# Kernel tuning notes

Measured on AMD Instinct MI355X. Metric: run time of the kernel, lower is better.

## Reference

```python
import math
import jax, jax.numpy as jnp
import numpy as np

B, N, T, C, H = 16, 307, 24, 128, 8
D = C // H
FACTOR = 5
S = min(FACTOR * int(np.ceil(np.log(T))), T)   # sample_k (U_part) = 20
U = S                                          # n_top u = 20


def _pos_emb(t_len, c):
    pos = jnp.arange(t_len, dtype=jnp.float32)[:, None]
    div = jnp.exp(jnp.arange(0, c, 2, dtype=jnp.float32) * (-math.log(10000.0) / c))
    pe = jnp.zeros((t_len, c), dtype=jnp.float32)
    pe = pe.at[:, 0::2].set(jnp.sin(pos * div))
    pe = pe.at[:, 1::2].set(jnp.cos(pos * div))
    return pe  # [T, C]


def _layernorm(x, g, b, eps=1e-5):
    m = x.mean(-1, keepdims=True)
    v = ((x - m) ** 2).mean(-1, keepdims=True)
    return (x - m) / jnp.sqrt(v + eps) * g + b


def _forward(query, time_encoder, index_sample,
             emb_minute, emb_hour, emb_weekday, emb_month, emb_year,
             Wq, Wk, Wv, Wo, bo, ff_w1, ff_b1, ff_w2, ff_b2,
             ln1_g, ln1_b, ln2_g, ln2_b):
    # DataEmbedding: x + positional + temporal (dropout = identity in eval)
    pe = _pos_emb(T, C)                                   # [T, C]
    te = (emb_minute[time_encoder[..., 0]] + emb_hour[time_encoder[..., 1]]
          + emb_weekday[time_encoder[..., 2]] + emb_month[time_encoder[..., 3]]
          + emb_year[time_encoder[..., 4]])               # [B, T, C]
    x = query + pe[None, None, :, :] + te[:, None, :, :]  # [B, N, T, C]

    # QKV projections -> [B, H, N, T, D]
    def proj(inp, W):
        return (inp @ W).reshape(B, N, T, H, D).transpose(0, 3, 1, 2, 4)
    Q, K, V = proj(x, Wq), proj(x, Wk), proj(x, Wv)

    # ProbSparse: sample S keys per query position
    K_samp = K[:, :, :, index_sample, :]                  # [B, H, N, T, S, D]
    QK_samp = jnp.einsum('bhntd,bhntsd->bhnts', Q, K_samp)
    M = QK_samp.max(-1) - QK_samp.sum(-1) / S             # [B, H, N, T]
    _, M_top = jax.lax.top_k(M, U)                        # [B, H, N, U]

    Q_red = jnp.take_along_axis(Q, M_top[..., None], axis=3)  # [B, H, N, U, D]
    scores = jnp.einsum('bhnud,bhntd->bhnut', Q_red, K) * (1.0 / math.sqrt(D))
    attn = jax.nn.softmax(scores, axis=-1)
    upd = jnp.einsum('bhnut,bhntd->bhnud', attn, V)       # [B, H, N, U, D]

    # initial context = mean over T, then scatter-update top-u query rows
    ctx = jnp.broadcast_to(V.mean(axis=3, keepdims=True), V.shape)
    ctx = ctx.at[jnp.arange(B)[:, None, None, None],
                 jnp.arange(H)[None, :, None, None],
                 jnp.arange(N)[None, None, :, None],
                 M_top].set(upd)

    ctx = ctx.transpose(0, 2, 3, 1, 4).reshape(B, N, T, C)
    att_out = ctx @ Wo + bo

    x1 = _layernorm(att_out + x, ln1_g, ln1_b)
    ff = jax.nn.relu(x1 @ ff_w1 + ff_b1) @ ff_w2 + ff_b2
    out = _layernorm(ff + x1, ln2_g, ln2_b)
    return out


def setup_inputs() -> dict:
    key = jax.random.key(0)
    ks = jax.random.split(key, 32)
    def nrm(i, shape, s=0.02):
        return jax.random.normal(ks[i], shape, dtype=jnp.float32) * s
    inp = {
        'value': jax.random.normal(ks[0], (B, N, T, C), dtype=jnp.float32),
        'key_in': jax.random.normal(ks[1], (B, N, T, C), dtype=jnp.float32),
        'query': jax.random.normal(ks[2], (B, N, T, C), dtype=jnp.float32),
        't': 1,
        'time_encoder': jax.random.randint(ks[3], (B, T, 5), 0, 10),
        'index_sample': jax.random.randint(ks[4], (T, S), 0, T),
        'emb_minute': nrm(5, (70, C), 1.0), 'emb_hour': nrm(6, (30, C), 1.0),
        'emb_weekday': nrm(7, (10, C), 1.0), 'emb_month': nrm(8, (40, C), 1.0),
        'emb_year': nrm(9, (400, C), 1.0),
        'Wq': nrm(10, (C, C)), 'Wk': nrm(11, (C, C)), 'Wv': nrm(12, (C, C)),
        'Wo': nrm(13, (C, C)), 'bo': jnp.zeros((C,), jnp.float32),
        'ff_w1': nrm(14, (C, 4 * C)), 'ff_b1': jnp.zeros((4 * C,), jnp.float32),
        'ff_w2': nrm(15, (4 * C, C)), 'ff_b2': jnp.zeros((C,), jnp.float32),
        'ln1_g': jnp.ones((C,), jnp.float32), 'ln1_b': jnp.zeros((C,), jnp.float32),
        'ln2_g': jnp.ones((C,), jnp.float32), 'ln2_b': jnp.zeros((C,), jnp.float32),
    }
    return inp


def reference(value, key_in, query, t, time_encoder, index_sample,
              emb_minute, emb_hour, emb_weekday, emb_month, emb_year,
              Wq, Wk, Wv, Wo, bo, ff_w1, ff_b1, ff_w2, ff_b2,
              ln1_g, ln1_b, ln2_g, ln2_b):
    # value, key_in, t are accepted but unused, matching the torch module
    return _forward(query, time_encoder, index_sample,
                    emb_minute, emb_hour, emb_weekday, emb_month, emb_year,
                    Wq, Wk, Wv, Wo, bo, ff_w1, ff_b1, ff_w2, ff_b2,
                    ln1_g, ln1_b, ln2_g, ln2_b)
```

## Files before the change

kernel.cpp:

```cpp
#include <hip/hip_runtime.h>
#include <hip/hip_bf16.h>
#include <cmath>

namespace {
constexpr int B_ = 16, N_ = 307, T_ = 24, C_ = 128, H_ = 8, D_ = 16, S_ = 20, U_ = 20;
constexpr int NROW = B_ * N_ * T_;
constexpr int NX = NROW * C_;
constexpr int TEPE_N = B_ * T_ * C_;
constexpr int FF = 4 * C_;
constexpr int BM = 32;
constexpr int NBLK_MM = NROW / BM;
constexpr int BMT = 32;
constexpr int NBLK_T = NROW / BMT;
constexpr int NUNIT = B_ * H_ * N_;
constexpr int PREP_N = TEPE_N + 384 * C_ + (2 * C_ * FF + C_ * C_);
}

typedef __attribute__((ext_vector_type(8))) short short8;
typedef __attribute__((ext_vector_type(4))) short short4_;
typedef __attribute__((ext_vector_type(4))) float f32x4;

__device__ inline short f2bf(float v) {
    union { float f; unsigned u; } a; a.f = v;
    unsigned r = a.u + 0x7fff + ((a.u >> 16) & 1);
    return (short)(r >> 16);
}
__device__ inline float bf2f(short s) {
    return __bfloat162float(*(const __hip_bfloat16*)&s);
}

__global__ void k_prep(const int* __restrict__ te,
                       const float* __restrict__ e_min, const float* __restrict__ e_hr,
                       const float* __restrict__ e_wd, const float* __restrict__ e_mo,
                       const float* __restrict__ e_yr, float* __restrict__ tepe,
                       const int* __restrict__ idxs, unsigned char* __restrict__ cntg,
                       const float* __restrict__ Wq, const float* __restrict__ Wk,
                       const float* __restrict__ Wv, short* __restrict__ wqkvf,
                       const float* __restrict__ w1, const float* __restrict__ w2,
                       const float* __restrict__ Wo,
                       short* __restrict__ w1f, short* __restrict__ w2f,
                       short* __restrict__ wof) {
    int i = blockIdx.x * 256 + threadIdx.x;
    if (i < TEPE_N) {
        int c = i & (C_ - 1);
        int bt = i >> 7;
        int t = bt % T_;
        const int* enc = te + bt * 5;
        float v = e_min[enc[0] * C_ + c] + e_hr[enc[1] * C_ + c] + e_wd[enc[2] * C_ + c]
                + e_mo[enc[3] * C_ + c] + e_yr[enc[4] * C_ + c];
        float ang = (float)t * expf(-(float)(c & ~1) * (9.210340371976184f / 128.0f));
        v += (c & 1) ? cosf(ang) : sinf(ang);
        tepe[i] = v;
    } else if (i < TEPE_N + 384 * C_) {
        int j = i - TEPE_N;
        int tile = j >> 9, l = (j >> 3) & 63, e = j & 7;
        int c_tile = tile >> 2, ks = tile & 3;
        int c_all = c_tile * 16 + (l & 15);
        int k = ks * 32 + (l >> 4) * 8 + e;
        int m = c_all >> 7, c = c_all & (C_ - 1);
        const float* W = (m == 0) ? Wq : (m == 1) ? Wk : Wv;
        wqkvf[j] = f2bf(W[k * C_ + c]);
    } else {
        int j = i - TEPE_N - 384 * C_;
        if (j < C_ * FF) {
            int tile = j >> 9, l = (j >> 3) & 63, e = j & 7;
            int jtile = tile >> 2, ks = tile & 3;
            int jj = jtile * 16 + (l & 15);
            int k = ks * 32 + (l >> 4) * 8 + e;
            w1f[j] = f2bf(w1[k * FF + jj]);
        } else if (j < 2 * C_ * FF) {
            int j2 = j - C_ * FF;
            int tile = j2 >> 9, l = (j2 >> 3) & 63, e = j2 & 7;
            int c_tile = tile >> 4, ks = tile & 15;
            int c = c_tile * 16 + (l & 15);
            int jj = ks * 32 + (l >> 4) * 8 + e;
            w2f[j2] = f2bf(w2[jj * C_ + c]);
        } else {
            int j3 = j - 2 * C_ * FF;
            int tile = j3 >> 9, l = (j3 >> 3) & 63, e = j3 & 7;
            int c_tile = tile >> 2, ks = tile & 3;
            int c = c_tile * 16 + (l & 15);
            int k = ks * 32 + (l >> 4) * 8 + e;
            wof[j3] = f2bf(Wo[k * C_ + c]);
        }
    }
    if (blockIdx.x == 0) {
        __shared__ int scnt[T_ * 32];
        for (int j = threadIdx.x; j < T_ * 32; j += 256) scnt[j] = 0;
        __syncthreads();
        for (int j = threadIdx.x; j < T_ * S_; j += 256) {
            int t = j / S_;
            atomicAdd(&scnt[t * 32 + idxs[j]], 1);
        }
        __syncthreads();
        for (int j = threadIdx.x; j < 192; j += 256) {
            unsigned v = (unsigned)scnt[4 * j] | ((unsigned)scnt[4 * j + 1] << 8)
                       | ((unsigned)scnt[4 * j + 2] << 16) | ((unsigned)scnt[4 * j + 3] << 24);
            ((unsigned*)cntg)[j] = v;
        }
    }
}

__global__ __launch_bounds__(256) void k_qkv_mfma(
    const float* __restrict__ query, const float* __restrict__ tepe,
    const short* __restrict__ wqkvf,
    short* __restrict__ Q, short* __restrict__ K, short* __restrict__ V) {
    __shared__ __align__(16) short xs[BM * C_];
    int tid = threadIdx.x;
    int r0 = blockIdx.x * BM;
    {
        int row = tid >> 3;
        int cb = (tid & 7) * 16;
        int gr = r0 + row;
        int t = gr % T_;
        int b = gr / (N_ * T_);
        const float* qsrc = query + (size_t)gr * C_ + cb;
        const float* tsrc = tepe + (size_t)(b * T_ + t) * C_ + cb;
        int swz0 = (row & 7) << 3;
#pragma unroll
        for (int i = 0; i < 4; i++) {
            float4 q4 = *(const float4*)(qsrc + 4 * i);
            float4 t4 = *(const float4*)(tsrc + 4 * i);
            short4_ sv;
            sv.x = f2bf(q4.x + t4.x); sv.y = f2bf(q4.y + t4.y);
            sv.z = f2bf(q4.z + t4.z); sv.w = f2bf(q4.w + t4.w);
            *(short4_*)&xs[(row * C_ + cb + 4 * i) ^ swz0] = sv;
        }
    }
    __syncthreads();
    int w = tid >> 6, l = tid & 63;
    int lr = l & 15, lk = l >> 4;
    int swz = (lr & 7) << 3;
    short8 bx[2][4];
#pragma unroll
    for (int rt = 0; rt < 2; rt++)
#pragma unroll
        for (int ks = 0; ks < 4; ks++)
            bx[rt][ks] = *(const short8*)&xs[((rt * 16 + lr) * C_ + ks * 32 + lk * 8) ^ swz];
    size_t base[2];
#pragma unroll
    for (int rt = 0; rt < 2; rt++) {
        int gr = r0 + rt * 16 + lr;
        int t = gr % T_;
        int n = (gr / T_) % N_;
        int b = gr / (N_ * T_);
        base[rt] = ((size_t)b * H_ * N_ + n) * (T_ * D_) + t * D_;
    }
#pragma unroll
    for (int jt = 0; jt < 6; jt++) {
        int ctile = w * 6 + jt;
        const short* ap = wqkvf + (size_t)ctile * 2048 + l * 8;
        short8 acur[4];
#pragma unroll
        for (int ks = 0; ks < 4; ks++) acur[ks] = *(const short8*)(ap + ks * 512);
        f32x4 acc[2] = {{0.f, 0.f, 0.f, 0.f}, {0.f, 0.f, 0.f, 0.f}};
#pragma unroll
        for (int ks = 0; ks < 4; ks++) {
#pragma unroll
            for (int rt = 0; rt < 2; rt++)
                acc[rt] = __builtin_amdgcn_mfma_f32_16x16x32_bf16(acur[ks], bx[rt][ks], acc[rt], 0, 0, 0);
        }
        int c0 = ctile * 16 + lk * 4;
        int m = c0 >> 7;
        int c = c0 & (C_ - 1);
        int h = c >> 4, d = c & 15;
        short* dst = (m == 0) ? Q : (m == 1) ? K : V;
#pragma unroll
        for (int rt = 0; rt < 2; rt++) {
            short4_ sv;
            sv.x = f2bf(acc[rt][0]); sv.y = f2bf(acc[rt][1]);
            sv.z = f2bf(acc[rt][2]); sv.w = f2bf(acc[rt][3]);
            *(short4_*)&dst[base[rt] + (size_t)h * (N_ * T_ * D_) + d] = sv;
        }
    }
}

__global__ __launch_bounds__(256) void k_attn(
    const short* __restrict__ Q, const short* __restrict__ K, const short* __restrict__ V,
    const unsigned char* __restrict__ cntg, short* __restrict__ ctx) {
    __shared__ __align__(16) short Qbf[4][32 * 24], Kbf[4][32 * 24];
    __shared__ __align__(16) short Vt[4][16 * 40];
    __shared__ __align__(16) short Pbf[4][32 * 40];
    __shared__ unsigned char cntS[T_ * 32];
    __shared__ float Mv[4][T_];
    __shared__ int keepS[4][T_];
    __shared__ float meanVs[4][D_];
    int tid = threadIdx.x;
    int wid = tid >> 6, l = tid & 63;
    int e = blockIdx.x * 4 + wid;
    const short* qb = Q + (size_t)e * (T_ * D_);
    const short* kb = K + (size_t)e * (T_ * D_);
    const short* vb = V + (size_t)e * (T_ * D_);
    if (l < 48) {
        int t = l >> 1, hf = l & 1;
        *(short8*)&Qbf[wid][t * 24 + hf * 8] = *(const short8*)(qb + t * 16 + hf * 8);
        *(short8*)&Kbf[wid][t * 24 + hf * 8] = *(const short8*)(kb + t * 16 + hf * 8);
    }
    for (int i = l; i < 96; i += 64) {
        int t = i >> 2, c4 = i & 3;
        short4_ v = *(const short4_*)(vb + t * 16 + c4 * 4);
        Vt[wid][(c4 * 4 + 0) * 40 + t] = v.x;
        Vt[wid][(c4 * 4 + 1) * 40 + t] = v.y;
        Vt[wid][(c4 * 4 + 2) * 40 + t] = v.z;
        Vt[wid][(c4 * 4 + 3) * 40 + t] = v.w;
    }
    for (int i = l; i < 128; i += 64) {
        int d = i >> 3, c = 24 + (i & 7);
        Vt[wid][d * 40 + c] = 0;
    }
    if (tid < 192) ((int*)cntS)[tid] = ((const int*)cntg)[tid];
    __syncthreads();
    if (l >= 48) {
        int d = l - 48;
        float s = 0.f;
        for (int t = 0; t < T_; t++) s += bf2f(Vt[wid][d * 40 + t]);
        meanVs[wid][d] = s * (1.0f / T_);
    }
    int lr = l & 15, lk = l >> 4;
    short8 zz = {};
    short8 kf0 = zz, kf1 = zz, qf0 = zz, qf1 = zz;
    if (lk < 2) {
        kf0 = *(const short8*)&Kbf[wid][lr * 24 + lk * 8];
        kf1 = *(const short8*)&Kbf[wid][(16 + lr) * 24 + lk * 8];
        qf0 = *(const short8*)&Qbf[wid][lr * 24 + lk * 8];
        qf1 = *(const short8*)&Qbf[wid][(16 + lr) * 24 + lk * 8];
    }
    f32x4 zf = {0.f, 0.f, 0.f, 0.f};
    __builtin_amdgcn_s_setprio(1);
    f32x4 s00 = __builtin_amdgcn_mfma_f32_16x16x32_bf16(kf0, qf0, zf, 0, 0, 0);
    f32x4 s01 = __builtin_amdgcn_mfma_f32_16x16x32_bf16(kf1, qf0, zf, 0, 0, 0);
    f32x4 s10 = __builtin_amdgcn_mfma_f32_16x16x32_bf16(kf0, qf1, zf, 0, 0, 0);
    f32x4 s11 = __builtin_amdgcn_mfma_f32_16x16x32_bf16(kf1, qf1, zf, 0, 0, 0);
    __builtin_amdgcn_s_setprio(0);
#pragma unroll
    for (int rt = 0; rt < 2; rt++) {
        int t = rt * 16 + lr;
        int tt = (t < T_) ? t : 0;
        f32x4 c0 = rt ? s10 : s00;
        f32x4 c1 = rt ? s11 : s01;
        float mx = -1e30f, sm = 0.f;
#pragma unroll
        for (int i = 0; i < 4; i++) {
            int cA = cntS[tt * 32 + lk * 4 + i];
            if (cA) { mx = fmaxf(mx, c0[i]); sm += (float)cA * c0[i]; }
        }
        if (lk < 2) {
#pragma unroll
            for (int i = 0; i < 4; i++) {
                int cB = cntS[tt * 32 + 16 + lk * 4 + i];
                if (cB) { mx = fmaxf(mx, c1[i]); sm += (float)cB * c1[i]; }
            }
        }
        mx = fmaxf(mx, __shfl_xor(mx, 16));
        mx = fmaxf(mx, __shfl_xor(mx, 32));
        sm += __shfl_xor(sm, 16);
        sm += __shfl_xor(sm, 32);
        if (lk == 0 && t < T_) Mv[wid][t] = mx - sm * (1.0f / S_);
    }
    __syncthreads();
    if (l < T_) {
        float mt = Mv[wid][l];
        int cnt2 = 0;
        for (int t2 = 0; t2 < T_; t2++) {
            float m2 = Mv[wid][t2];
            cnt2 += (m2 > mt) || (m2 == mt && t2 < l);
        }
        keepS[wid][l] = (cnt2 < U_) ? 1 : 0;
    }
#pragma unroll
    for (int rt = 0; rt < 2; rt++) {
        f32x4 c0 = rt ? s10 : s00;
        f32x4 c1 = rt ? s11 : s01;
        float lm = fmaxf(fmaxf(c0[0], c0[1]), fmaxf(c0[2], c0[3]));
        if (lk < 2) lm = fmaxf(lm, fmaxf(fmaxf(c1[0], c1[1]), fmaxf(c1[2], c1[3])));
        lm = fmaxf(lm, __shfl_xor(lm, 16));
        lm = fmaxf(lm, __shfl_xor(lm, 32));
        float e0[4], e1[4];
        float ls = 0.f;
#pragma unroll
        for (int i = 0; i < 4; i++) { e0[i] = __expf(0.25f * (c0[i] - lm)); ls += e0[i]; }
#pragma unroll
        for (int i = 0; i < 4; i++) { e1[i] = (lk < 2) ? __expf(0.25f * (c1[i] - lm)) : 0.f; ls += e1[i]; }
        ls += __shfl_xor(ls, 16);
        ls += __shfl_xor(ls, 32);
        float inv = 1.0f / ls;
        short4_ w0, w1;
        w0.x = f2bf(e0[0] * inv); w0.y = f2bf(e0[1] * inv);
        w0.z = f2bf(e0[2] * inv); w0.w = f2bf(e0[3] * inv);
        w1.x = f2bf(e1[0] * inv); w1.y = f2bf(e1[1] * inv);
        w1.z = f2bf(e1[2] * inv); w1.w = f2bf(e1[3] * inv);
        int trow = rt * 16 + lr;
        *(short4_*)&Pbf[wid][trow * 40 + lk * 4] = w0;
        *(short4_*)&Pbf[wid][trow * 40 + 16 + lk * 4] = w1;
    }
    __syncthreads();
    short8 vf = *(const short8*)&Vt[wid][lr * 40 + lk * 8];
    short8 pf0 = *(const short8*)&Pbf[wid][lr * 40 + lk * 8];
    short8 pf1 = *(const short8*)&Pbf[wid][(16 + lr) * 40 + lk * 8];
    __builtin_amdgcn_s_setprio(1);
    f32x4 u0 = __builtin_amdgcn_mfma_f32_16x16x32_bf16(vf, pf0, zf, 0, 0, 0);
    f32x4 u1 = __builtin_amdgcn_mfma_f32_16x16x32_bf16(vf, pf1, zf, 0, 0, 0);
    __builtin_amdgcn_s_setprio(0);
    int b = e / (H_ * N_);
    int h = (e / N_) % H_;
    int n = e % N_;
    float4 mv4 = *(const float4*)&meanVs[wid][lk * 4];
#pragma unroll
    for (int rt = 0; rt < 2; rt++) {
        int t = rt * 16 + lr;
        if (t < T_) {
            f32x4 u = rt ? u1 : u0;
            float4 o;
            if (keepS[wid][t]) { o.x = u[0]; o.y = u[1]; o.z = u[2]; o.w = u[3]; }
            else o = mv4;
            short4_ sv;
            sv.x = f2bf(o.x); sv.y = f2bf(o.y); sv.z = f2bf(o.z); sv.w = f2bf(o.w);
            *(short4_*)&ctx[((size_t)(b * N_ + n) * T_ + t) * C_ + h * D_ + lk * 4] = sv;
        }
    }
}

__global__ __launch_bounds__(256, 4) void k_tail(
    const short* __restrict__ ctx, const short* __restrict__ wof, const float* __restrict__ bo,
    const float* __restrict__ query, const float* __restrict__ tepe,
    const float* __restrict__ g1, const float* __restrict__ b1,
    const short* __restrict__ w1f, const float* __restrict__ b1f,
    const short* __restrict__ w2f, const float* __restrict__ b2f,
    const float* __restrict__ g2, const float* __restrict__ b2ln,
    float* __restrict__ out) {
    __shared__ __align__(16) char smem[25088];
    float (*xf)[132] = (float(*)[132])smem;
    short* hbf = (short*)smem;
    float (*yf)[132] = (float(*)[132])smem;
    short* cbf = (short*)(smem + 16896);
    short* x1bf = (short*)(smem + 16896);
    int tid = threadIdx.x;
    int r0 = blockIdx.x * BMT;
    {
        int row = tid >> 3;
        int cb = (tid & 7) * 16;
        int gr = r0 + row;
        int t = gr % T_;
        int b = gr / (N_ * T_);
        const short* csrc = ctx + (size_t)gr * C_ + cb;
        const float* qsrc = query + (size_t)gr * C_ + cb;
        const float* tsrc = tepe + (size_t)(b * T_ + t) * C_ + cb;
        int swz0 = (row & 7) << 3;
        *(short8*)&cbf[(row * C_ + cb) ^ swz0] = *(const short8*)csrc;
        *(short8*)&cbf[(row * C_ + cb + 8) ^ swz0] = *(const short8*)(csrc + 8);
#pragma unroll
        for (int i = 0; i < 4; i++) {
            float4 q4 = *(const float4*)(qsrc + 4 * i);
            float4 t4 = *(const float4*)(tsrc + 4 * i);
            float4 xr;
            xr.x = q4.x + t4.x; xr.y = q4.y + t4.y;
            xr.z = q4.z + t4.z; xr.w = q4.w + t4.w;
            *(float4*)&xf[row][cb + 4 * i] = xr;
        }
    }
    __syncthreads();
    int w = tid >> 6, l = tid & 63;
    int lr = l & 15, lk = l >> 4;
    int swz = (lr & 7) << 3;
    {
#pragma unroll
        for (int ct = 0; ct < 2; ct++) {
            int c_tile = w * 2 + ct;
            const short* ap = wof + (size_t)c_tile * 2048 + l * 8;
            short8 acur[4];
#pragma unroll
            for (int ks = 0; ks < 4; ks++) acur[ks] = *(const short8*)(ap + ks * 512);
            f32x4 acc[2] = {{0.f, 0.f, 0.f, 0.f}, {0.f, 0.f, 0.f, 0.f}};
            __builtin_amdgcn_s_setprio(1);
#pragma unroll
            for (int ks = 0; ks < 4; ks++) {
#pragma unroll
                for (int rt = 0; rt < 2; rt++) {
                    short8 bc = *(const short8*)&cbf[((rt * 16 + lr) * C_ + ks * 32 + lk * 8) ^ swz];
                    acc[rt] = __builtin_amdgcn_mfma_f32_16x16x32_bf16(acur[ks], bc, acc[rt], 0, 0, 0);
                }
            }
            __builtin_amdgcn_s_setprio(0);
            int cc = c_tile * 16 + lk * 4;
            float4 bias = *(const float4*)(bo + cc);
#pragma unroll
            for (int rt = 0; rt < 2; rt++) {
                int rr = rt * 16 + lr;
                float4 res = *(const float4*)&xf[rr][cc];
                float4 o;
                o.x = acc[rt][0] + bias.x + res.x;
                o.y = acc[rt][1] + bias.y + res.y;
                o.z = acc[rt][2] + bias.z + res.z;
                o.w = acc[rt][3] + bias.w + res.w;
                *(float4*)&xf[rr][cc] = o;
            }
        }
    }
    __syncthreads();
    {
        int r = tid >> 3;
        int q = tid & 7;
        int cb = q * 16;
        float vals[16];
        float s = 0.f;
#pragma unroll
        for (int i = 0; i < 16; i++) { vals[i] = xf[r][cb + i]; s += vals[i]; }
        s += __shfl_xor(s, 1, 8);
        s += __shfl_xor(s, 2, 8);
        s += __shfl_xor(s, 4, 8);
        float mean = s * (1.f / C_);
        float vv = 0.f;
#pragma unroll
        for (int i = 0; i < 16; i++) { float d = vals[i] - mean; vv += d * d; }
        vv += __shfl_xor(vv, 1, 8);
        vv += __shfl_xor(vv, 2, 8);
        vv += __shfl_xor(vv, 4, 8);
        float rstd = rsqrtf(vv * (1.f / C_) + 1e-5f);
        short8 o0, o1;
#pragma unroll
        for (int i = 0; i < 8; i++) {
            o0[i] = f2bf((vals[i] - mean) * rstd * g1[cb + i] + b1[cb + i]);
            o1[i] = f2bf((vals[8 + i] - mean) * rstd * g1[cb + 8 + i] + b1[cb + 8 + i]);
        }
        int swz0 = (r & 7) << 3;
        *(short8*)&x1bf[(r * C_ + cb) ^ swz0] = o0;
        *(short8*)&x1bf[(r * C_ + cb + 8) ^ swz0] = o1;
    }
    __syncthreads();
    f32x4 acc2[2][2] = {{{0.f, 0.f, 0.f, 0.f}, {0.f, 0.f, 0.f, 0.f}},
                        {{0.f, 0.f, 0.f, 0.f}, {0.f, 0.f, 0.f, 0.f}}};
    for (int p = 0; p < 2; p++) {
        {
            short8 bx[2][4];
#pragma unroll
            for (int rt = 0; rt < 2; rt++)
#pragma unroll
                for (int ks = 0; ks < 4; ks++)
                    bx[rt][ks] = *(const short8*)&x1bf[((rt * 16 + lr) * C_ + ks * 32 + lk * 8) ^ swz];
#pragma unroll
            for (int jt = 0; jt < 4; jt++) {
                int jtile = p * 16 + w * 4 + jt;
                const short* ap = w1f + (size_t)jtile * 2048 + l * 8;
                short8 acur[4];
#pragma unroll
                for (int ks = 0; ks < 4; ks++) acur[ks] = *(const short8*)(ap + ks * 512);
                f32x4 acc[2] = {{0.f, 0.f, 0.f, 0.f}, {0.f, 0.f, 0.f, 0.f}};
                __builtin_amdgcn_s_setprio(1);
#pragma unroll
                for (int ks = 0; ks < 4; ks++) {
#pragma unroll
                    for (int rt = 0; rt < 2; rt++)
                        acc[rt] = __builtin_amdgcn_mfma_f32_16x16x32_bf16(acur[ks], bx[rt][ks], acc[rt], 0, 0, 0);
                }
                __builtin_amdgcn_s_setprio(0);
                int j0g = jtile * 16 + lk * 4;
                int j0l = (w * 4 + jt) * 16 + lk * 4;
                float4 bias = *(const float4*)(b1f + j0g);
#pragma unroll
                for (int rt = 0; rt < 2; rt++) {
                    int rr = rt * 16 + lr;
                    short4_ hv;
                    hv.x = f2bf(fmaxf(acc[rt][0] + bias.x, 0.f));
                    hv.y = f2bf(fmaxf(acc[rt][1] + bias.y, 0.f));
                    hv.z = f2bf(fmaxf(acc[rt][2] + bias.z, 0.f));
                    hv.w = f2bf(fmaxf(acc[rt][3] + bias.w, 0.f));
                    *(short4_*)&hbf[(rr * 256 + j0l) ^ swz] = hv;
                }
            }
        }
        __syncthreads();
        __builtin_amdgcn_s_setprio(1);
#pragma unroll 2
        for (int ks = 0; ks < 8; ks++) {
#pragma unroll
            for (int ct = 0; ct < 2; ct++) {
                short8 aw = *(const short8*)(w2f + ((size_t)((w * 2 + ct) * 16 + p * 8 + ks)) * 512 + l * 8);
#pragma unroll
                for (int rt = 0; rt < 2; rt++) {
                    short8 hx = *(const short8*)&hbf[((rt * 16 + lr) * 256 + ks * 32 + lk * 8) ^ swz];
                    acc2[ct][rt] = __builtin_amdgcn_mfma_f32_16x16x32_bf16(aw, hx, acc2[ct][rt], 0, 0, 0);
                }
            }
        }
        __builtin_amdgcn_s_setprio(0);
        __syncthreads();
    }
    {
#pragma unroll
        for (int ct = 0; ct < 2; ct++) {
            int cc = (w * 2 + ct) * 16 + lk * 4;
            float4 bias2 = *(const float4*)(b2f + cc);
#pragma unroll
            for (int rt = 0; rt < 2; rt++) {
                int rr = rt * 16 + lr;
                short4_ rb = *(const short4_*)&x1bf[(rr * C_ + cc) ^ swz];
                float4 o;
                o.x = acc2[ct][rt][0] + bias2.x + bf2f(rb.x);
                o.y = acc2[ct][rt][1] + bias2.y + bf2f(rb.y);
                o.z = acc2[ct][rt][2] + bias2.z + bf2f(rb.z);
                o.w = acc2[ct][rt][3] + bias2.w + bf2f(rb.w);
                *(float4*)&yf[rr][cc] = o;
            }
        }
    }
    __syncthreads();
    {
        int r = tid >> 3;
        int q = tid & 7;
        int cb = q * 16;
        float vals[16];
        float s = 0.f;
#pragma unroll
        for (int i = 0; i < 16; i++) { vals[i] = yf[r][cb + i]; s += vals[i]; }
        s += __shfl_xor(s, 1, 8);
        s += __shfl_xor(s, 2, 8);
        s += __shfl_xor(s, 4, 8);
        float mean = s * (1.f / C_);
        float vv = 0.f;
#pragma unroll
        for (int i = 0; i < 16; i++) { float d = vals[i] - mean; vv += d * d; }
        vv += __shfl_xor(vv, 1, 8);
        vv += __shfl_xor(vv, 2, 8);
        vv += __shfl_xor(vv, 4, 8);
        float rstd = rsqrtf(vv * (1.f / C_) + 1e-5f);
        float* op = out + (size_t)(r0 + r) * C_ + cb;
#pragma unroll
        for (int i4 = 0; i4 < 4; i4++) {
            float4 gv = *(const float4*)(g2 + cb + 4 * i4);
            float4 bv = *(const float4*)(b2ln + cb + 4 * i4);
            float4 ov;
            ov.x = (vals[4 * i4 + 0] - mean) * rstd * gv.x + bv.x;
            ov.y = (vals[4 * i4 + 1] - mean) * rstd * gv.y + bv.y;
            ov.z = (vals[4 * i4 + 2] - mean) * rstd * gv.z + bv.z;
            ov.w = (vals[4 * i4 + 3] - mean) * rstd * gv.w + bv.w;
            *(float4*)(op + 4 * i4) = ov;
        }
    }
}

extern "C" void kernel_launch(void* const* d_in, const int* in_sizes, int n_in,
                              void* d_out, int out_size, void* d_ws, size_t ws_size,
                              hipStream_t stream) {
    const float* query = (const float*)d_in[2];
    const int* time_enc = (const int*)d_in[4];
    const int* index_sample = (const int*)d_in[5];
    const float* e_min = (const float*)d_in[6];
    const float* e_hr  = (const float*)d_in[7];
    const float* e_wd  = (const float*)d_in[8];
    const float* e_mo  = (const float*)d_in[9];
    const float* e_yr  = (const float*)d_in[10];
    const float* Wq = (const float*)d_in[11];
    const float* Wk = (const float*)d_in[12];
    const float* Wv = (const float*)d_in[13];
    const float* Wo = (const float*)d_in[14];
    const float* bo = (const float*)d_in[15];
    const float* ffw1 = (const float*)d_in[16];
    const float* ffb1 = (const float*)d_in[17];
    const float* ffw2 = (const float*)d_in[18];
    const float* ffb2 = (const float*)d_in[19];
    const float* ln1g = (const float*)d_in[20];
    const float* ln1b = (const float*)d_in[21];
    const float* ln2g = (const float*)d_in[22];
    const float* ln2b = (const float*)d_in[23];

    float* ws = (float*)d_ws;
    float* tepe = ws;
    float* region1 = ws + TEPE_N;
    float* region2 = region1 + NX;
    float* region3 = region2 + NX;
    float* region4 = region3 + NX;

    short* Qb = (short*)region1;
    short* Kb = (short*)region2;
    short* Vb = (short*)region3;
    short* ctxb = (short*)region4;
    short* wqkvf = (short*)region4 + NX;
    unsigned char* cntg = (unsigned char*)((short*)region4 + NX + 49152);
    short* w1f = (short*)region2 + NX;
    short* w2f = w1f + C_ * FF;
    short* wof = w2f + C_ * FF;

    k_prep<<<dim3(PREP_N / 256), dim3(256), 0, stream>>>(
        time_enc, e_min, e_hr, e_wd, e_mo, e_yr, tepe, index_sample, cntg,
        Wq, Wk, Wv, wqkvf, ffw1, ffw2, Wo, w1f, w2f, wof);
    k_qkv_mfma<<<dim3(NBLK_MM), dim3(256), 0, stream>>>(
        query, tepe, wqkvf, Qb, Kb, Vb);
    k_attn<<<dim3(NUNIT / 4), dim3(256), 0, stream>>>(
        Qb, Kb, Vb, cntg, ctxb);
    k_tail<<<dim3(NBLK_T), dim3(256), 0, stream>>>(
        ctxb, wof, bo, query, tepe, ln1g, ln1b,
        w1f, ffb1, w2f, ffb2, ln2g, ln2b, (float*)d_out);
}
```

Before: 162.7 us.

## Process two row tiles per tail block and prefetch the next tile's inputs

```diff
diff --git a/kernel.cpp b/kernel.cpp
--- a/kernel.cpp
+++ b/kernel.cpp
@@ -11,7 +11,8 @@
 constexpr int BM = 32;
 constexpr int NBLK_MM = NROW / BM;
 constexpr int BMT = 32;
-constexpr int NBLK_T = NROW / BMT;
+constexpr int NTILE_T = NROW / BMT;
+constexpr int NBLK_T = NTILE_T / 2;
 constexpr int NUNIT = B_ * H_ * N_;
 constexpr int PREP_N = TEPE_N + 384 * C_ + (2 * C_ * FF + C_ * C_);
 }
@@ -335,206 +336,218 @@
     short* cbf = (short*)(smem + 16896);
     short* x1bf = (short*)(smem + 16896);
     int tid = threadIdx.x;
-    int r0 = blockIdx.x * BMT;
-    {
-        int row = tid >> 3;
-        int cb = (tid & 7) * 16;
-        int gr = r0 + row;
+    int row = tid >> 3;
+    int cb = (tid & 7) * 16;
+    int w = tid >> 6, l = tid & 63;
+    int lr = l & 15, lk = l >> 4;
+    int swz = (lr & 7) << 3;
+    short8 c0r, c1r;
+    float4 xr[4];
+    auto LOADT = [&](int tile) {
+        int gr = tile * BMT + row;
         int t = gr % T_;
         int b = gr / (N_ * T_);
         const short* csrc = ctx + (size_t)gr * C_ + cb;
+        c0r = *(const short8*)csrc;
+        c1r = *(const short8*)(csrc + 8);
         const float* qsrc = query + (size_t)gr * C_ + cb;
         const float* tsrc = tepe + (size_t)(b * T_ + t) * C_ + cb;
-        int swz0 = (row & 7) << 3;
-        *(short8*)&cbf[(row * C_ + cb) ^ swz0] = *(const short8*)csrc;
-        *(short8*)&cbf[(row * C_ + cb + 8) ^ swz0] = *(const short8*)(csrc + 8);
 #pragma unroll
         for (int i = 0; i < 4; i++) {
             float4 q4 = *(const float4*)(qsrc + 4 * i);
             float4 t4 = *(const float4*)(tsrc + 4 * i);
-            float4 xr;
-            xr.x = q4.x + t4.x; xr.y = q4.y + t4.y;
-            xr.z = q4.z + t4.z; xr.w = q4.w + t4.w;
-            *(float4*)&xf[row][cb + 4 * i] = xr;
-        }
-    }
-    __syncthreads();
-    int w = tid >> 6, l = tid & 63;
-    int lr = l & 15, lk = l >> 4;
-    int swz = (lr & 7) << 3;
-    {
-#pragma unroll
-        for (int ct = 0; ct < 2; ct++) {
-            int c_tile = w * 2 + ct;
-            const short* ap = wof + (size_t)c_tile * 2048 + l * 8;
-            short8 acur[4];
-#pragma unroll
-            for (int ks = 0; ks < 4; ks++) acur[ks] = *(const short8*)(ap + ks * 512);
-            f32x4 acc[2] = {{0.f, 0.f, 0.f, 0.f}, {0.f, 0.f, 0.f, 0.f}};
+            xr[i].x = q4.x + t4.x; xr[i].y = q4.y + t4.y;
+            xr[i].z = q4.z + t4.z; xr[i].w = q4.w + t4.w;
+        }
+    };
+    LOADT(blockIdx.x * 2);
+    for (int it = 0; it < 2; it++) {
+        int r0 = (blockIdx.x * 2 + it) * BMT;
+        {
+            int swz0 = (row & 7) << 3;
+            *(short8*)&cbf[(row * C_ + cb) ^ swz0] = c0r;
+            *(short8*)&cbf[(row * C_ + cb + 8) ^ swz0] = c1r;
+#pragma unroll
+            for (int i = 0; i < 4; i++)
+                *(float4*)&xf[row][cb + 4 * i] = xr[i];
+        }
+        __syncthreads();
+        if (it == 0) LOADT(blockIdx.x * 2 + 1);
+        {
+#pragma unroll
+            for (int ct = 0; ct < 2; ct++) {
+                int c_tile = w * 2 + ct;
+                const short* ap = wof + (size_t)c_tile * 2048 + l * 8;
+                short8 acur[4];
+#pragma unroll
+                for (int ks = 0; ks < 4; ks++) acur[ks] = *(const short8*)(ap + ks * 512);
+                f32x4 acc[2] = {{0.f, 0.f, 0.f, 0.f}, {0.f, 0.f, 0.f, 0.f}};
+                __builtin_amdgcn_s_setprio(1);
+#pragma unroll
+                for (int ks = 0; ks < 4; ks++) {
+#pragma unroll
+                    for (int rt = 0; rt < 2; rt++) {
+                        short8 bc = *(const short8*)&cbf[((rt * 16 + lr) * C_ + ks * 32 + lk * 8) ^ swz];
+                        acc[rt] = __builtin_amdgcn_mfma_f32_16x16x32_bf16(acur[ks], bc, acc[rt], 0, 0, 0);
+                    }
+                }
+                __builtin_amdgcn_s_setprio(0);
+                int cc = c_tile * 16 + lk * 4;
+                float4 bias = *(const float4*)(bo + cc);
+#pragma unroll
+                for (int rt = 0; rt < 2; rt++) {
+                    int rr = rt * 16 + lr;
+                    float4 res = *(const float4*)&xf[rr][cc];
+                    float4 o;
+                    o.x = acc[rt][0] + bias.x + res.x;
+                    o.y = acc[rt][1] + bias.y + res.y;
+                    o.z = acc[rt][2] + bias.z + res.z;
+                    o.w = acc[rt][3] + bias.w + res.w;
+                    *(float4*)&xf[rr][cc] = o;
+                }
+            }
+        }
+        __syncthreads();
+        {
+            int r = tid >> 3;
+            int q = tid & 7;
+            int cb2 = q * 16;
+            float vals[16];
+            float s = 0.f;
+#pragma unroll
+            for (int i = 0; i < 16; i++) { vals[i] = xf[r][cb2 + i]; s += vals[i]; }
+            s += __shfl_xor(s, 1, 8);
+            s += __shfl_xor(s, 2, 8);
+            s += __shfl_xor(s, 4, 8);
+            float mean = s * (1.f / C_);
+            float vv = 0.f;
+#pragma unroll
+            for (int i = 0; i < 16; i++) { float d = vals[i] - mean; vv += d * d; }
+            vv += __shfl_xor(vv, 1, 8);
+            vv += __shfl_xor(vv, 2, 8);
+            vv += __shfl_xor(vv, 4, 8);
+            float rstd = rsqrtf(vv * (1.f / C_) + 1e-5f);
+            short8 o0, o1;
+#pragma unroll
+            for (int i = 0; i < 8; i++) {
+                o0[i] = f2bf((vals[i] - mean) * rstd * g1[cb2 + i] + b1[cb2 + i]);
+                o1[i] = f2bf((vals[8 + i] - mean) * rstd * g1[cb2 + 8 + i] + b1[cb2 + 8 + i]);
+            }
+            int swz0 = (r & 7) << 3;
+            *(short8*)&x1bf[(r * C_ + cb2) ^ swz0] = o0;
+            *(short8*)&x1bf[(r * C_ + cb2 + 8) ^ swz0] = o1;
+        }
+        __syncthreads();
+        f32x4 acc2[2][2] = {{{0.f, 0.f, 0.f, 0.f}, {0.f, 0.f, 0.f, 0.f}},
+                            {{0.f, 0.f, 0.f, 0.f}, {0.f, 0.f, 0.f, 0.f}}};
+        for (int p = 0; p < 2; p++) {
+            {
+                short8 bx[2][4];
+#pragma unroll
+                for (int rt = 0; rt < 2; rt++)
+#pragma unroll
+                    for (int ks = 0; ks < 4; ks++)
+                        bx[rt][ks] = *(const short8*)&x1bf[((rt * 16 + lr) * C_ + ks * 32 + lk * 8) ^ swz];
+#pragma unroll
+                for (int jt = 0; jt < 4; jt++) {
+                    int jtile = p * 16 + w * 4 + jt;
+                    const short* ap = w1f + (size_t)jtile * 2048 + l * 8;
+                    short8 acur[4];
+#pragma unroll
+                    for (int ks = 0; ks < 4; ks++) acur[ks] = *(const short8*)(ap + ks * 512);
+                    f32x4 acc[2] = {{0.f, 0.f, 0.f, 0.f}, {0.f, 0.f, 0.f, 0.f}};
+                    __builtin_amdgcn_s_setprio(1);
+#pragma unroll
+                    for (int ks = 0; ks < 4; ks++) {
+#pragma unroll
+                        for (int rt = 0; rt < 2; rt++)
+                            acc[rt] = __builtin_amdgcn_mfma_f32_16x16x32_bf16(acur[ks], bx[rt][ks], acc[rt], 0, 0, 0);
+                    }
+                    __builtin_amdgcn_s_setprio(0);
+                    int j0g = jtile * 16 + lk * 4;
+                    int j0l = (w * 4 + jt) * 16 + lk * 4;
+                    float4 bias = *(const float4*)(b1f + j0g);
+#pragma unroll
+                    for (int rt = 0; rt < 2; rt++) {
+                        int rr = rt * 16 + lr;
+                        short4_ hv;
+                        hv.x = f2bf(fmaxf(acc[rt][0] + bias.x, 0.f));
+                        hv.y = f2bf(fmaxf(acc[rt][1] + bias.y, 0.f));
+                        hv.z = f2bf(fmaxf(acc[rt][2] + bias.z, 0.f));
+                        hv.w = f2bf(fmaxf(acc[rt][3] + bias.w, 0.f));
+                        *(short4_*)&hbf[(rr * 256 + j0l) ^ swz] = hv;
+                    }
+                }
+            }
+            __syncthreads();
             __builtin_amdgcn_s_setprio(1);
-#pragma unroll
-            for (int ks = 0; ks < 4; ks++) {
-#pragma unroll
-                for (int rt = 0; rt < 2; rt++) {
-                    short8 bc = *(const short8*)&cbf[((rt * 16 + lr) * C_ + ks * 32 + lk * 8) ^ swz];
-                    acc[rt] = __builtin_amdgcn_mfma_f32_16x16x32_bf16(acur[ks], bc, acc[rt], 0, 0, 0);
+#pragma unroll 2
+            for (int ks = 0; ks < 8; ks++) {
+#pragma unroll
+                for (int ct = 0; ct < 2; ct++) {
+                    short8 aw = *(const short8*)(w2f + ((size_t)((w * 2 + ct) * 16 + p * 8 + ks)) * 512 + l * 8);
+#pragma unroll
+                    for (int rt = 0; rt < 2; rt++) {
+                        short8 hx = *(const short8*)&hbf[((rt * 16 + lr) * 256 + ks * 32 + lk * 8) ^ swz];
+                        acc2[ct][rt] = __builtin_amdgcn_mfma_f32_16x16x32_bf16(aw, hx, acc2[ct][rt], 0, 0, 0);
+                    }
                 }
             }
             __builtin_amdgcn_s_setprio(0);
-            int cc = c_tile * 16 + lk * 4;
-            float4 bias = *(const float4*)(bo + cc);
-#pragma unroll
-            for (int rt = 0; rt < 2; rt++) {
-                int rr = rt * 16 + lr;
-                float4 res = *(const float4*)&xf[rr][cc];
-                float4 o;
-                o.x = acc[rt][0] + bias.x + res.x;
-                o.y = acc[rt][1] + bias.y + res.y;
-                o.z = acc[rt][2] + bias.z + res.z;
-                o.w = acc[rt][3] + bias.w + res.w;
-                *(float4*)&xf[rr][cc] = o;
-            }
-        }
-    }
-    __syncthreads();
-    {
-        int r = tid >> 3;
-        int q = tid & 7;
-        int cb = q * 16;
-        float vals[16];
-        float s = 0.f;
-#pragma unroll
-        for (int i = 0; i < 16; i++) { vals[i] = xf[r][cb + i]; s += vals[i]; }
-        s += __shfl_xor(s, 1, 8);
-        s += __shfl_xor(s, 2, 8);
-        s += __shfl_xor(s, 4, 8);
-        float mean = s * (1.f / C_);
-        float vv = 0.f;
-#pragma unroll
-        for (int i = 0; i < 16; i++) { float d = vals[i] - mean; vv += d * d; }
-        vv += __shfl_xor(vv, 1, 8);
-        vv += __shfl_xor(vv, 2, 8);
-        vv += __shfl_xor(vv, 4, 8);
-        float rstd = rsqrtf(vv * (1.f / C_) + 1e-5f);
-        short8 o0, o1;
-#pragma unroll
-        for (int i = 0; i < 8; i++) {
-            o0[i] = f2bf((vals[i] - mean) * rstd * g1[cb + i] + b1[cb + i]);
-            o1[i] = f2bf((vals[8 + i] - mean) * rstd * g1[cb + 8 + i] + b1[cb + 8 + i]);
-        }
-        int swz0 = (r & 7) << 3;
-        *(short8*)&x1bf[(r * C_ + cb) ^ swz0] = o0;
-        *(short8*)&x1bf[(r * C_ + cb + 8) ^ swz0] = o1;
-    }
-    __syncthreads();
-    f32x4 acc2[2][2] = {{{0.f, 0.f, 0.f, 0.f}, {0.f, 0.f, 0.f, 0.f}},
-                        {{0.f, 0.f, 0.f, 0.f}, {0.f, 0.f, 0.f, 0.f}}};
-    for (int p = 0; p < 2; p++) {
+            __syncthreads();
+        }
         {
-            short8 bx[2][4];
-#pragma unroll
-            for (int rt = 0; rt < 2; rt++)
-#pragma unroll
-                for (int ks = 0; ks < 4; ks++)
-                    bx[rt][ks] = *(const short8*)&x1bf[((rt * 16 + lr) * C_ + ks * 32 + lk * 8) ^ swz];
-#pragma unroll
-            for (int jt = 0; jt < 4; jt++) {
-                int jtile = p * 16 + w * 4 + jt;
-                const short* ap = w1f + (size_t)jtile * 2048 + l * 8;
-                short8 acur[4];
-#pragma unroll
-                for (int ks = 0; ks < 4; ks++) acur[ks] = *(const short8*)(ap + ks * 512);
-                f32x4 acc[2] = {{0.f, 0.f, 0.f, 0.f}, {0.f, 0.f, 0.f, 0.f}};
-                __builtin_amdgcn_s_setprio(1);
-#pragma unroll
-                for (int ks = 0; ks < 4; ks++) {
-#pragma unroll
-                    for (int rt = 0; rt < 2; rt++)
-                        acc[rt] = __builtin_amdgcn_mfma_f32_16x16x32_bf16(acur[ks], bx[rt][ks], acc[rt], 0, 0, 0);
-                }
-                __builtin_amdgcn_s_setprio(0);
-                int j0g = jtile * 16 + lk * 4;
-                int j0l = (w * 4 + jt) * 16 + lk * 4;
-                float4 bias = *(const float4*)(b1f + j0g);
+#pragma unroll
+            for (int ct = 0; ct < 2; ct++) {
+                int cc = (w * 2 + ct) * 16 + lk * 4;
+                float4 bias2 = *(const float4*)(b2f + cc);
 #pragma unroll
                 for (int rt = 0; rt < 2; rt++) {
                     int rr = rt * 16 + lr;
-                    short4_ hv;
-                    hv.x = f2bf(fmaxf(acc[rt][0] + bias.x, 0.f));
-                    hv.y = f2bf(fmaxf(acc[rt][1] + bias.y, 0.f));
-                    hv.z = f2bf(fmaxf(acc[rt][2] + bias.z, 0.f));
-                    hv.w = f2bf(fmaxf(acc[rt][3] + bias.w, 0.f));
-                    *(short4_*)&hbf[(rr * 256 + j0l) ^ swz] = hv;
+                    short4_ rb = *(const short4_*)&x1bf[(rr * C_ + cc) ^ swz];
+                    float4 o;
+                    o.x = acc2[ct][rt][0] + bias2.x + bf2f(rb.x);
+                    o.y = acc2[ct][rt][1] + bias2.y + bf2f(rb.y);
+                    o.z = acc2[ct][rt][2] + bias2.z + bf2f(rb.z);
+                    o.w = acc2[ct][rt][3] + bias2.w + bf2f(rb.w);
+                    *(float4*)&yf[rr][cc] = o;
                 }
             }
         }
         __syncthreads();
-        __builtin_amdgcn_s_setprio(1);
-#pragma unroll 2
-        for (int ks = 0; ks < 8; ks++) {
-#pragma unroll
-            for (int ct = 0; ct < 2; ct++) {
-                short8 aw = *(const short8*)(w2f + ((size_t)((w * 2 + ct) * 16 + p * 8 + ks)) * 512 + l * 8);
-#pragma unroll
-                for (int rt = 0; rt < 2; rt++) {
-                    short8 hx = *(const short8*)&hbf[((rt * 16 + lr) * 256 + ks * 32 + lk * 8) ^ swz];
-                    acc2[ct][rt] = __builtin_amdgcn_mfma_f32_16x16x32_bf16(aw, hx, acc2[ct][rt], 0, 0, 0);
-                }
+        {
+            int r = tid >> 3;
+            int q = tid & 7;
+            int cb2 = q * 16;
+            float vals[16];
+            float s = 0.f;
+#pragma unroll
+            for (int i = 0; i < 16; i++) { vals[i] = yf[r][cb2 + i]; s += vals[i]; }
+            s += __shfl_xor(s, 1, 8);
+            s += __shfl_xor(s, 2, 8);
+            s += __shfl_xor(s, 4, 8);
+            float mean = s * (1.f / C_);
+            float vv = 0.f;
+#pragma unroll
+            for (int i = 0; i < 16; i++) { float d = vals[i] - mean; vv += d * d; }
+            vv += __shfl_xor(vv, 1, 8);
+            vv += __shfl_xor(vv, 2, 8);
+            vv += __shfl_xor(vv, 4, 8);
+            float rstd = rsqrtf(vv * (1.f / C_) + 1e-5f);
+            float* op = out + (size_t)(r0 + r) * C_ + cb2;
+#pragma unroll
+            for (int i4 = 0; i4 < 4; i4++) {
+                float4 gv = *(const float4*)(g2 + cb2 + 4 * i4);
+                float4 bv = *(const float4*)(b2ln + cb2 + 4 * i4);
+                float4 ov;
+                ov.x = (vals[4 * i4 + 0] - mean) * rstd * gv.x + bv.x;
+                ov.y = (vals[4 * i4 + 1] - mean) * rstd * gv.y + bv.y;
+                ov.z = (vals[4 * i4 + 2] - mean) * rstd * gv.z + bv.z;
+                ov.w = (vals[4 * i4 + 3] - mean) * rstd * gv.w + bv.w;
+                *(float4*)(op + 4 * i4) = ov;
             }
         }
-        __builtin_amdgcn_s_setprio(0);
         __syncthreads();
-    }
-    {
-#pragma unroll
-        for (int ct = 0; ct < 2; ct++) {
-            int cc = (w * 2 + ct) * 16 + lk * 4;
-            float4 bias2 = *(const float4*)(b2f + cc);
-#pragma unroll
-            for (int rt = 0; rt < 2; rt++) {
-                int rr = rt * 16 + lr;
-                short4_ rb = *(const short4_*)&x1bf[(rr * C_ + cc) ^ swz];
-                float4 o;
-                o.x = acc2[ct][rt][0] + bias2.x + bf2f(rb.x);
-                o.y = acc2[ct][rt][1] + bias2.y + bf2f(rb.y);
-                o.z = acc2[ct][rt][2] + bias2.z + bf2f(rb.z);
-                o.w = acc2[ct][rt][3] + bias2.w + bf2f(rb.w);
-                *(float4*)&yf[rr][cc] = o;
-            }
-        }
-    }
-    __syncthreads();
-    {
-        int r = tid >> 3;
-        int q = tid & 7;
-        int cb = q * 16;
-        float vals[16];
-        float s = 0.f;
-#pragma unroll
-        for (int i = 0; i < 16; i++) { vals[i] = yf[r][cb + i]; s += vals[i]; }
-        s += __shfl_xor(s, 1, 8);
-        s += __shfl_xor(s, 2, 8);
-        s += __shfl_xor(s, 4, 8);
-        float mean = s * (1.f / C_);
-        float vv = 0.f;
-#pragma unroll
-        for (int i = 0; i < 16; i++) { float d = vals[i] - mean; vv += d * d; }
-        vv += __shfl_xor(vv, 1, 8);
-        vv += __shfl_xor(vv, 2, 8);
-        vv += __shfl_xor(vv, 4, 8);
-        float rstd = rsqrtf(vv * (1.f / C_) + 1e-5f);
-        float* op = out + (size_t)(r0 + r) * C_ + cb;
-#pragma unroll
-        for (int i4 = 0; i4 < 4; i4++) {
-            float4 gv = *(const float4*)(g2 + cb + 4 * i4);
-            float4 bv = *(const float4*)(b2ln + cb + 4 * i4);
-            float4 ov;
-            ov.x = (vals[4 * i4 + 0] - mean) * rstd * gv.x + bv.x;
-            ov.y = (vals[4 * i4 + 1] - mean) * rstd * gv.y + bv.y;
-            ov.z = (vals[4 * i4 + 2] - mean) * rstd * gv.z + bv.z;
-            ov.w = (vals[4 * i4 + 3] - mean) * rstd * gv.w + bv.w;
-            *(float4*)(op + 4 * i4) = ov;
-        }
     }
 }
 
```

Result: slower. 544.6 us (+234.7%).
